# Performance work log

Hardware: AMD Instinct MI355X
Metric: run time of the kernel (lower is better)

Reference implementation:

```python
import jax, jax.numpy as jnp
import numpy as np

NEAR = 0.01
FAR = 10.0
MAX_ITERS = 32
N_RAYS = 65536
HIDDEN = 128


def setup_inputs() -> dict:
    key = jax.random.key(0)
    ks = jax.random.split(key, 12)
    f = jnp.float32
    origins = jax.random.normal(ks[0], (N_RAYS, 3), f) * 2.0
    directions = jax.random.normal(ks[1], (N_RAYS, 3), f)
    directions = directions / jnp.linalg.norm(directions, axis=-1, keepdims=True)
    s1 = 1.0 / np.sqrt(3.0)
    s2 = 1.0 / np.sqrt(HIDDEN)
    return {
        "origins": origins,
        "directions": directions,
        "W1": jax.random.normal(ks[2], (3, HIDDEN), f) * s1,
        "b1": jax.random.normal(ks[3], (HIDDEN,), f) * 0.01,
        "W2": jax.random.normal(ks[4], (HIDDEN, HIDDEN), f) * s2,
        "b2": jax.random.normal(ks[5], (HIDDEN,), f) * 0.01,
        "W3": jax.random.normal(ks[6], (HIDDEN, 1), f) * s2,
        "b3": jax.random.normal(ks[7], (1,), f) * 0.01,
        "Wc1": jax.random.normal(ks[8], (3, HIDDEN), f) * s1,
        "bc1": jax.random.normal(ks[9], (HIDDEN,), f) * 0.01,
        "Wc2": jax.random.normal(ks[10], (HIDDEN, 3), f) * s2,
        "bc2": jax.random.normal(ks[11], (3,), f) * 0.01,
    }


def reference(origins, directions, W1, b1, W2, b2, W3, b3, Wc1, bc1, Wc2, bc2):
    N = origins.shape[0]

    def sdf(p):  # [N,3] -> [N,1]
        h = jax.nn.relu(p @ W1 + b1)
        h = jax.nn.relu(h @ W2 + b2)
        return h @ W3 + b3

    def get_color(p):  # [N,3] -> [N,3]
        h = jax.nn.relu(p @ Wc1 + bc1)
        return jax.nn.sigmoid(h @ Wc2 + bc2)

    def step(state, _):
        points, distances, final_mask = state
        sdfs = sdf(points)                                  # [N,1]
        valid = (sdfs <= NEAR) & (distances < FAR)          # [N,1] bool
        final_mask = final_mask | valid
        upd = ~valid                                        # rays still marching
        distances = distances + jnp.where(upd, sdfs, 0.0)
        points = points + jnp.where(upd, directions * sdfs, 0.0)
        return (points, distances, final_mask), None

    init = (origins,
            jnp.zeros((N, 1), origins.dtype),
            jnp.zeros((N, 1), dtype=bool))
    (points, distances, final_mask), _ = jax.lax.scan(step, init, None, length=MAX_ITERS)
    final_mask = final_mask | (distances < FAR)             # [N,1]

    # color[mask] = get_color(points[mask]) <=> masked where (get_color is pointwise)
    color = jnp.where(final_mask, get_color(points), 0.0)   # [N,3]
    return color
```

## Files before the change

### kernel.cpp

```cpp
#include <hip/hip_runtime.h>

#define HIDDEN 128
#define N_RAYS 65536
#define NEAR_D 0.01f
#define FAR_D 10.0f
#define MAX_ITERS 32

typedef _Float16 f16x8 __attribute__((ext_vector_type(8)));
typedef float f32x16 __attribute__((ext_vector_type(16)));

template <int CTRL, int ROW_MASK>
__device__ __forceinline__ float dpp_add(float v) {
    int s = __builtin_amdgcn_update_dpp(0, __float_as_int(v), CTRL, ROW_MASK, 0xF, true);
    return v + __int_as_float(s);
}
__device__ __forceinline__ float half_sum_dpp(float v) {
    v = dpp_add<0x111, 0xF>(v);
    v = dpp_add<0x112, 0xF>(v);
    v = dpp_add<0x114, 0xF>(v);
    v = dpp_add<0x118, 0xF>(v);
    v = dpp_add<0x142, 0xA>(v);
    return v;
}

__global__ void w2_frag_kernel(const float* __restrict__ W2,
                               _Float16* __restrict__ img) {
    int tid = blockIdx.x * blockDim.x + threadIdx.x;
    int j = tid & 7;
    int L = (tid >> 3) & 63;
    int tc = tid >> 9;
    int t = tc >> 3, c = tc & 7;
    int n = t * 32 + (L & 31);
    int k = c * 16 + ((L >> 5) & 1) * 8 + j;
    float w = W2[k * HIDDEN + n];
    _Float16 hi = (_Float16)w;
    _Float16 lo = (_Float16)(w - (float)hi);
    img[tid] = hi;
    img[16384 + tid] = lo;
}

__launch_bounds__(256, 2)
__global__ void sphere_trace_kernel(
    const float* __restrict__ origins,
    const float* __restrict__ directions,
    const float* __restrict__ W1,
    const float* __restrict__ b1,
    const _Float16* __restrict__ w2img,
    const float* __restrict__ b2,
    const float* __restrict__ W3,
    const float* __restrict__ b3,
    const float* __restrict__ Wc1,
    const float* __restrict__ bc1,
    const float* __restrict__ Wc2,
    const float* __restrict__ bc2,
    float* __restrict__ out)
{
    __shared__ __align__(16) _Float16 wlds[32768];
    __shared__ __align__(16) float4 w1s[128];
    __shared__ float sbuf[4][32];

    const int tid = threadIdx.x;
    const int lane = tid & 63;
    const int w = __builtin_amdgcn_readfirstlane(tid >> 6);
    const int q = lane >> 5;
    const int n32 = lane & 31;

    {
        const float4* src = (const float4*)w2img;
        float4* dst = (float4*)wlds;
        #pragma unroll
        for (int i = 0; i < 16; ++i)
            dst[tid + 256 * i] = src[tid + 256 * i];
        if (tid < 128) {
            float4 wv;
            wv.x = W1[tid];
            wv.y = W1[HIDDEN + tid];
            wv.z = W1[2 * HIDDEN + tid];
            wv.w = b1[tid];
            w1s[tid] = wv;
        }
    }
    __syncthreads();

    float bAx, bAy, bAz, bB;
    {
        bAx = fmaxf(fabsf(W1[lane]),              fabsf(W1[lane + 64]));
        bAy = fmaxf(fabsf(W1[HIDDEN + lane]),     fabsf(W1[HIDDEN + lane + 64]));
        bAz = fmaxf(fabsf(W1[2 * HIDDEN + lane]), fabsf(W1[2 * HIDDEN + lane + 64]));
        bB  = fmaxf(fabsf(b1[lane]),              fabsf(b1[lane + 64]));
        #pragma unroll
        for (int m = 1; m < 64; m <<= 1) {
            bAx = fmaxf(bAx, __shfl_xor(bAx, m));
            bAy = fmaxf(bAy, __shfl_xor(bAy, m));
            bAz = fmaxf(bAz, __shfl_xor(bAz, m));
            bB  = fmaxf(bB,  __shfl_xor(bB,  m));
        }
    }

    const int ray = blockIdx.x * 128 + w * 32 + n32;
    float px = origins[ray * 3 + 0];
    float py = origins[ray * 3 + 1];
    float pz = origins[ray * 3 + 2];
    const float dx = directions[ray * 3 + 0];
    const float dy = directions[ray * 3 + 1];
    const float dz = directions[ray * 3 + 2];
    float dist = 0.0f;
    bool frozen = false;

    float b2v[4], w3v[4];
    #pragma unroll
    for (int t = 0; t < 4; ++t) {
        b2v[t] = b2[t * 32 + n32];
        w3v[t] = W3[t * 32 + n32];
    }
    const float b3v = b3[0];
    const int q8 = q * 8;

    #pragma unroll 1
    for (int it = 0; it < MAX_ITERS; ++it) {
        const float ppx = px;
        const float ppy = py;
        const float ppz = pz;

        const float bound = fmaf(fabsf(ppx), bAx, fmaf(fabsf(ppy), bAy,
                            fmaf(fabsf(ppz), bAz, bB)));
        float sc = 1.0f, inv = 1.0f;
        {
            const int e = (int)((__float_as_uint(bound) >> 23) & 255u);
            if (e > 137) {
                const int sh = e - 137;
                sc  = __uint_as_float((unsigned)(127 - sh) << 23);
                inv = __uint_as_float((unsigned)(127 + sh) << 23);
            }
        }

        auto layer1 = [&](int kb, f16x8& Ah, f16x8& Al) {
            #pragma unroll
            for (int jj = 0; jj < 8; ++jj) {
                const float4 wv = w1s[kb + jj];
                const float hv = fmaxf(
                    fmaf(ppx, wv.x, fmaf(ppy, wv.y,
                    fmaf(ppz, wv.z, wv.w))), 0.0f);
                const float x = hv * sc;
                const _Float16 hi = (_Float16)x;
                Ah[jj] = hi;
                Al[jj] = (_Float16)(x - (float)hi);
            }
        };

        f32x16 acc[4];
        #pragma unroll
        for (int t = 0; t < 4; ++t)
            #pragma unroll
            for (int r = 0; r < 16; ++r) acc[t][r] = 0.0f;

        f16x8 Ah, Al, AhN, AlN;
        layer1(q8, Ah, Al);

        #pragma unroll 1
        for (int c = 0; c < 8; ++c) {
            const int base = (c << 9) + (lane << 3);
            const f16x8 b0h = *(const f16x8*)(wlds + base);
            const f16x8 b0l = *(const f16x8*)(wlds + 16384 + base);
            const f16x8 b1h = *(const f16x8*)(wlds + base + (1 << 12));
            const f16x8 b1l = *(const f16x8*)(wlds + 16384 + base + (1 << 12));
            const f16x8 b2h = *(const f16x8*)(wlds + base + (2 << 12));
            const f16x8 b2l = *(const f16x8*)(wlds + 16384 + base + (2 << 12));
            const f16x8 b3h = *(const f16x8*)(wlds + base + (3 << 12));
            const f16x8 b3l = *(const f16x8*)(wlds + 16384 + base + (3 << 12));

            if (c < 7) layer1((c + 1) * 16 + q8, AhN, AlN);

            __builtin_amdgcn_s_setprio(1);
            acc[0] = __builtin_amdgcn_mfma_f32_32x32x16_f16(Ah, b0h, acc[0], 0, 0, 0);
            acc[1] = __builtin_amdgcn_mfma_f32_32x32x16_f16(Ah, b1h, acc[1], 0, 0, 0);
            acc[2] = __builtin_amdgcn_mfma_f32_32x32x16_f16(Ah, b2h, acc[2], 0, 0, 0);
            acc[3] = __builtin_amdgcn_mfma_f32_32x32x16_f16(Ah, b3h, acc[3], 0, 0, 0);
            acc[0] = __builtin_amdgcn_mfma_f32_32x32x16_f16(Ah, b0l, acc[0], 0, 0, 0);
            acc[1] = __builtin_amdgcn_mfma_f32_32x32x16_f16(Ah, b1l, acc[1], 0, 0, 0);
            acc[2] = __builtin_amdgcn_mfma_f32_32x32x16_f16(Ah, b2l, acc[2], 0, 0, 0);
            acc[3] = __builtin_amdgcn_mfma_f32_32x32x16_f16(Ah, b3l, acc[3], 0, 0, 0);
            acc[0] = __builtin_amdgcn_mfma_f32_32x32x16_f16(Al, b0h, acc[0], 0, 0, 0);
            acc[1] = __builtin_amdgcn_mfma_f32_32x32x16_f16(Al, b1h, acc[1], 0, 0, 0);
            acc[2] = __builtin_amdgcn_mfma_f32_32x32x16_f16(Al, b2h, acc[2], 0, 0, 0);
            acc[3] = __builtin_amdgcn_mfma_f32_32x32x16_f16(Al, b3h, acc[3], 0, 0, 0);
            __builtin_amdgcn_s_setprio(0);

            Ah = AhN; Al = AlN;
        }

        float invr[16];
        #pragma unroll
        for (int r = 0; r < 16; ++r) {
            const int m0 = (r & 3) + 8 * (r >> 2);
            const float ilo = __uint_as_float(
                (unsigned)__builtin_amdgcn_readlane(__float_as_uint(inv), m0));
            const float ihi = __uint_as_float(
                (unsigned)__builtin_amdgcn_readlane(__float_as_uint(inv), m0 + 4));
            invr[r] = q ? ihi : ilo;
        }
        float ps[16];
        #pragma unroll
        for (int r = 0; r < 16; ++r) ps[r] = 0.0f;
        #pragma unroll
        for (int t = 0; t < 4; ++t) {
            #pragma unroll
            for (int r = 0; r < 16; ++r) {
                const float v = fmaxf(fmaf(acc[t][r], invr[r], b2v[t]), 0.0f);
                ps[r] = fmaf(v, w3v[t], ps[r]);
            }
        }

        #pragma unroll
        for (int r = 0; r < 16; ++r)
            ps[r] = half_sum_dpp(ps[r]);
        if ((lane & 31) == 31) {
            const int mb = q * 4;
            #pragma unroll
            for (int g = 0; g < 4; ++g) {
                float4 v4;
                v4.x = ps[4 * g + 0];
                v4.y = ps[4 * g + 1];
                v4.z = ps[4 * g + 2];
                v4.w = ps[4 * g + 3];
                *(float4*)&sbuf[w][8 * g + mb] = v4;
            }
        }
        const float s = sbuf[w][n32] + b3v;

        {
            const bool valid = (s <= NEAR_D) && (dist < FAR_D);
            if (!frozen) {
                if (valid) {
                    frozen = true;
                } else {
                    dist += s;
                    px = fmaf(dx, s, px);
                    py = fmaf(dy, s, py);
                    pz = fmaf(dz, s, pz);
                }
            }
        }
        if (__ballot((lane < 32) && !frozen) == 0) break;
    }

    const int k0 = lane, k1 = lane + 64;
    const float cx0 = Wc1[k0], cx1 = Wc1[k1];
    const float cy0 = Wc1[HIDDEN + k0], cy1 = Wc1[HIDDEN + k1];
    const float cz0 = Wc1[2 * HIDDEN + k0], cz1 = Wc1[2 * HIDDEN + k1];
    const float cb0 = bc1[k0], cb1 = bc1[k1];
    const float u00 = Wc2[k0 * 3 + 0], u01 = Wc2[k0 * 3 + 1], u02 = Wc2[k0 * 3 + 2];
    const float u10 = Wc2[k1 * 3 + 0], u11 = Wc2[k1 * 3 + 1], u12 = Wc2[k1 * 3 + 2];

    float g0 = 0.f, g1 = 0.f, g2 = 0.f;
    #pragma unroll 1
    for (int m = 0; m < 32; ++m) {
        const float qx = __shfl(px, m);
        const float qy = __shfl(py, m);
        const float qz = __shfl(pz, m);
        const float h0 = fmaxf(fmaf(qx, cx0, fmaf(qy, cy0, fmaf(qz, cz0, cb0))), 0.f);
        const float h1 = fmaxf(fmaf(qx, cx1, fmaf(qy, cy1, fmaf(qz, cz1, cb1))), 0.f);
        float a0 = fmaf(h0, u00, h1 * u10);
        float a1 = fmaf(h0, u01, h1 * u11);
        float a2 = fmaf(h0, u02, h1 * u12);
        #pragma unroll
        for (int mask = 1; mask < 64; mask <<= 1) {
            a0 += __shfl_xor(a0, mask);
            a1 += __shfl_xor(a1, mask);
            a2 += __shfl_xor(a2, mask);
        }
        if (lane == m) { g0 = a0; g1 = a1; g2 = a2; }
    }

    if (lane < 32) {
        float c0 = 0.f, c1 = 0.f, c2 = 0.f;
        if (frozen || dist < FAR_D) {
            c0 = 1.0f / (1.0f + __expf(-(g0 + bc2[0])));
            c1 = 1.0f / (1.0f + __expf(-(g1 + bc2[1])));
            c2 = 1.0f / (1.0f + __expf(-(g2 + bc2[2])));
        }
        out[ray * 3 + 0] = c0;
        out[ray * 3 + 1] = c1;
        out[ray * 3 + 2] = c2;
    }
}

extern "C" void kernel_launch(void* const* d_in, const int* in_sizes, int n_in,
                              void* d_out, int out_size, void* d_ws, size_t ws_size,
                              hipStream_t stream) {
    const float* origins    = (const float*)d_in[0];
    const float* directions = (const float*)d_in[1];
    const float* W1  = (const float*)d_in[2];
    const float* b1  = (const float*)d_in[3];
    const float* W2  = (const float*)d_in[4];
    const float* b2  = (const float*)d_in[5];
    const float* W3  = (const float*)d_in[6];
    const float* b3  = (const float*)d_in[7];
    const float* Wc1 = (const float*)d_in[8];
    const float* bc1 = (const float*)d_in[9];
    const float* Wc2 = (const float*)d_in[10];
    const float* bc2 = (const float*)d_in[11];
    float* out = (float*)d_out;

    _Float16* w2img = (_Float16*)d_ws;

    w2_frag_kernel<<<64, 256, 0, stream>>>(W2, w2img);

    sphere_trace_kernel<<<N_RAYS / 128, 256, 0, stream>>>(
        origins, directions, W1, b1, w2img, b2, W3, b3,
        Wc1, bc1, Wc2, bc2, out);
}
```

Before: 315.5 us.

## Split each ray group's layer-2 N dimension across two waves, low weights from global

Each block now handles 64 rays, and each 32-ray group is processed by two waves. Each wave computes half of the hidden-2 outputs and the partial SDF sums are combined through shared memory with block-wide syncs. Only the high-half fp16 weights stay in LDS; the low half is streamed from global/L2, which halves LDS use and allows 4 blocks per CU. The trade-offs are that layer 1 is now computed redundantly by both waves, there is a __syncthreads every iteration, the early exit is block-wide, and the color stage leaves half the waves idle.

```diff
diff --git a/kernel.cpp b/kernel.cpp
--- a/kernel.cpp
+++ b/kernel.cpp
@@ -39,7 +39,7 @@
     img[16384 + tid] = lo;
 }
 
-__launch_bounds__(256, 2)
+__launch_bounds__(256, 4)
 __global__ void sphere_trace_kernel(
     const float* __restrict__ origins,
     const float* __restrict__ directions,
@@ -55,29 +55,31 @@
     const float* __restrict__ bc2,
     float* __restrict__ out)
 {
-    __shared__ __align__(16) _Float16 wlds[32768];
+    __shared__ __align__(16) _Float16 whi[16384];
     __shared__ __align__(16) float4 w1s[128];
-    __shared__ float sbuf[4][32];
+    __shared__ float sbuf[2][2][32];
 
     const int tid = threadIdx.x;
     const int lane = tid & 63;
-    const int w = __builtin_amdgcn_readfirstlane(tid >> 6);
+    const int wv  = __builtin_amdgcn_readfirstlane(tid >> 6);
+    const int grp = wv >> 1;
+    const int th  = wv & 1;
     const int q = lane >> 5;
     const int n32 = lane & 31;
 
     {
         const float4* src = (const float4*)w2img;
-        float4* dst = (float4*)wlds;
+        float4* dst = (float4*)whi;
         #pragma unroll
-        for (int i = 0; i < 16; ++i)
+        for (int i = 0; i < 8; ++i)
             dst[tid + 256 * i] = src[tid + 256 * i];
         if (tid < 128) {
-            float4 wv;
-            wv.x = W1[tid];
-            wv.y = W1[HIDDEN + tid];
-            wv.z = W1[2 * HIDDEN + tid];
-            wv.w = b1[tid];
-            w1s[tid] = wv;
+            float4 wvv;
+            wvv.x = W1[tid];
+            wvv.y = W1[HIDDEN + tid];
+            wvv.z = W1[2 * HIDDEN + tid];
+            wvv.w = b1[tid];
+            w1s[tid] = wvv;
         }
     }
     __syncthreads();
@@ -97,7 +99,7 @@
         }
     }
 
-    const int ray = blockIdx.x * 128 + w * 32 + n32;
+    const int ray = blockIdx.x * 64 + grp * 32 + n32;
     float px = origins[ray * 3 + 0];
     float py = origins[ray * 3 + 1];
     float pz = origins[ray * 3 + 2];
@@ -107,128 +109,117 @@
     float dist = 0.0f;
     bool frozen = false;
 
-    float b2v[4], w3v[4];
+    const int t0 = th * 2;
+    float b2v[2], w3v[2];
     #pragma unroll
-    for (int t = 0; t < 4; ++t) {
-        b2v[t] = b2[t * 32 + n32];
-        w3v[t] = W3[t * 32 + n32];
+    for (int tt = 0; tt < 2; ++tt) {
+        b2v[tt] = b2[(t0 + tt) * 32 + n32];
+        w3v[tt] = W3[(t0 + tt) * 32 + n32];
     }
     const float b3v = b3[0];
     const int q8 = q * 8;
+    const int fb0 = t0 * 8;
+    const int fb1 = fb0 + 8;
+    const _Float16* lo_base  = w2img + 16384 + (lane << 3);
+    const _Float16* whi_lane = whi + (lane << 3);
 
     #pragma unroll 1
     for (int it = 0; it < MAX_ITERS; ++it) {
-        const float ppx = px;
-        const float ppy = py;
-        const float ppz = pz;
-
-        const float bound = fmaf(fabsf(ppx), bAx, fmaf(fabsf(ppy), bAy,
-                            fmaf(fabsf(ppz), bAz, bB)));
-        float sc = 1.0f, inv = 1.0f;
-        {
-            const int e = (int)((__float_as_uint(bound) >> 23) & 255u);
-            if (e > 137) {
-                const int sh = e - 137;
-                sc  = __uint_as_float((unsigned)(127 - sh) << 23);
-                inv = __uint_as_float((unsigned)(127 + sh) << 23);
-            }
-        }
-
-        auto layer1 = [&](int kb, f16x8& Ah, f16x8& Al) {
-            #pragma unroll
-            for (int jj = 0; jj < 8; ++jj) {
-                const float4 wv = w1s[kb + jj];
-                const float hv = fmaxf(
-                    fmaf(ppx, wv.x, fmaf(ppy, wv.y,
-                    fmaf(ppz, wv.z, wv.w))), 0.0f);
-                const float x = hv * sc;
-                const _Float16 hi = (_Float16)x;
-                Ah[jj] = hi;
-                Al[jj] = (_Float16)(x - (float)hi);
-            }
-        };
-
-        f32x16 acc[4];
-        #pragma unroll
-        for (int t = 0; t < 4; ++t)
-            #pragma unroll
-            for (int r = 0; r < 16; ++r) acc[t][r] = 0.0f;
-
-        f16x8 Ah, Al, AhN, AlN;
-        layer1(q8, Ah, Al);
-
-        #pragma unroll 1
-        for (int c = 0; c < 8; ++c) {
-            const int base = (c << 9) + (lane << 3);
-            const f16x8 b0h = *(const f16x8*)(wlds + base);
-            const f16x8 b0l = *(const f16x8*)(wlds + 16384 + base);
-            const f16x8 b1h = *(const f16x8*)(wlds + base + (1 << 12));
-            const f16x8 b1l = *(const f16x8*)(wlds + 16384 + base + (1 << 12));
-            const f16x8 b2h = *(const f16x8*)(wlds + base + (2 << 12));
-            const f16x8 b2l = *(const f16x8*)(wlds + 16384 + base + (2 << 12));
-            const f16x8 b3h = *(const f16x8*)(wlds + base + (3 << 12));
-            const f16x8 b3l = *(const f16x8*)(wlds + 16384 + base + (3 << 12));
-
-            if (c < 7) layer1((c + 1) * 16 + q8, AhN, AlN);
-
-            __builtin_amdgcn_s_setprio(1);
-            acc[0] = __builtin_amdgcn_mfma_f32_32x32x16_f16(Ah, b0h, acc[0], 0, 0, 0);
-            acc[1] = __builtin_amdgcn_mfma_f32_32x32x16_f16(Ah, b1h, acc[1], 0, 0, 0);
-            acc[2] = __builtin_amdgcn_mfma_f32_32x32x16_f16(Ah, b2h, acc[2], 0, 0, 0);
-            acc[3] = __builtin_amdgcn_mfma_f32_32x32x16_f16(Ah, b3h, acc[3], 0, 0, 0);
-            acc[0] = __builtin_amdgcn_mfma_f32_32x32x16_f16(Ah, b0l, acc[0], 0, 0, 0);
-            acc[1] = __builtin_amdgcn_mfma_f32_32x32x16_f16(Ah, b1l, acc[1], 0, 0, 0);
-            acc[2] = __builtin_amdgcn_mfma_f32_32x32x16_f16(Ah, b2l, acc[2], 0, 0, 0);
-            acc[3] = __builtin_amdgcn_mfma_f32_32x32x16_f16(Ah, b3l, acc[3], 0, 0, 0);
-            acc[0] = __builtin_amdgcn_mfma_f32_32x32x16_f16(Al, b0h, acc[0], 0, 0, 0);
-            acc[1] = __builtin_amdgcn_mfma_f32_32x32x16_f16(Al, b1h, acc[1], 0, 0, 0);
-            acc[2] = __builtin_amdgcn_mfma_f32_32x32x16_f16(Al, b2h, acc[2], 0, 0, 0);
-            acc[3] = __builtin_amdgcn_mfma_f32_32x32x16_f16(Al, b3h, acc[3], 0, 0, 0);
-            __builtin_amdgcn_s_setprio(0);
-
-            Ah = AhN; Al = AlN;
-        }
-
-        float invr[16];
-        #pragma unroll
-        for (int r = 0; r < 16; ++r) {
-            const int m0 = (r & 3) + 8 * (r >> 2);
-            const float ilo = __uint_as_float(
-                (unsigned)__builtin_amdgcn_readlane(__float_as_uint(inv), m0));
-            const float ihi = __uint_as_float(
-                (unsigned)__builtin_amdgcn_readlane(__float_as_uint(inv), m0 + 4));
-            invr[r] = q ? ihi : ilo;
-        }
-        float ps[16];
-        #pragma unroll
-        for (int r = 0; r < 16; ++r) ps[r] = 0.0f;
-        #pragma unroll
-        for (int t = 0; t < 4; ++t) {
+        const bool gdone = (__ballot(!frozen) == 0ull);
+        if (!gdone) {
+            const float ppx = px, ppy = py, ppz = pz;
+
+            const float bound = fmaf(fabsf(ppx), bAx, fmaf(fabsf(ppy), bAy,
+                                fmaf(fabsf(ppz), bAz, bB)));
+            float sc = 1.0f, inv = 1.0f;
+            {
+                const int e = (int)((__float_as_uint(bound) >> 23) & 255u);
+                if (e > 137) {
+                    const int sh = e - 137;
+                    sc  = __uint_as_float((unsigned)(127 - sh) << 23);
+                    inv = __uint_as_float((unsigned)(127 + sh) << 23);
+                }
+            }
+
+            f32x16 acc0, acc1;
+            #pragma unroll
+            for (int r = 0; r < 16; ++r) { acc0[r] = 0.0f; acc1[r] = 0.0f; }
+
+            f16x8 Bl0 = *(const f16x8*)(lo_base + (fb0 << 9));
+            f16x8 Bl1 = *(const f16x8*)(lo_base + (fb1 << 9));
+
+            #pragma unroll 1
+            for (int c = 0; c < 8; ++c) {
+                const f16x8 bh0 = *(const f16x8*)(whi_lane + ((fb0 + c) << 9));
+                const f16x8 bh1 = *(const f16x8*)(whi_lane + ((fb1 + c) << 9));
+                f16x8 BlN0, BlN1;
+                if (c < 7) {
+                    BlN0 = *(const f16x8*)(lo_base + ((fb0 + c + 1) << 9));
+                    BlN1 = *(const f16x8*)(lo_base + ((fb1 + c + 1) << 9));
+                }
+                f16x8 Ah, Al;
+                {
+                    const int kb = c * 16 + q8;
+                    #pragma unroll
+                    for (int jj = 0; jj < 8; ++jj) {
+                        const float4 wvv = w1s[kb + jj];
+                        const float hv = fmaxf(
+                            fmaf(ppx, wvv.x, fmaf(ppy, wvv.y,
+                            fmaf(ppz, wvv.z, wvv.w))), 0.0f);
+                        const float x = hv * sc;
+                        const _Float16 hi = (_Float16)x;
+                        Ah[jj] = hi;
+                        Al[jj] = (_Float16)(x - (float)hi);
+                    }
+                }
+                __builtin_amdgcn_s_setprio(1);
+                acc0 = __builtin_amdgcn_mfma_f32_32x32x16_f16(Ah, bh0, acc0, 0, 0, 0);
+                acc1 = __builtin_amdgcn_mfma_f32_32x32x16_f16(Ah, bh1, acc1, 0, 0, 0);
+                acc0 = __builtin_amdgcn_mfma_f32_32x32x16_f16(Ah, Bl0, acc0, 0, 0, 0);
+                acc1 = __builtin_amdgcn_mfma_f32_32x32x16_f16(Ah, Bl1, acc1, 0, 0, 0);
+                acc0 = __builtin_amdgcn_mfma_f32_32x32x16_f16(Al, bh0, acc0, 0, 0, 0);
+                acc1 = __builtin_amdgcn_mfma_f32_32x32x16_f16(Al, bh1, acc1, 0, 0, 0);
+                __builtin_amdgcn_s_setprio(0);
+                if (c < 7) { Bl0 = BlN0; Bl1 = BlN1; }
+            }
+
+            float invr[16];
             #pragma unroll
             for (int r = 0; r < 16; ++r) {
-                const float v = fmaxf(fmaf(acc[t][r], invr[r], b2v[t]), 0.0f);
-                ps[r] = fmaf(v, w3v[t], ps[r]);
-            }
-        }
-
-        #pragma unroll
-        for (int r = 0; r < 16; ++r)
-            ps[r] = half_sum_dpp(ps[r]);
-        if ((lane & 31) == 31) {
-            const int mb = q * 4;
-            #pragma unroll
-            for (int g = 0; g < 4; ++g) {
-                float4 v4;
-                v4.x = ps[4 * g + 0];
-                v4.y = ps[4 * g + 1];
-                v4.z = ps[4 * g + 2];
-                v4.w = ps[4 * g + 3];
-                *(float4*)&sbuf[w][8 * g + mb] = v4;
-            }
-        }
-        const float s = sbuf[w][n32] + b3v;
-
-        {
+                const int m0 = (r & 3) + 8 * (r >> 2);
+                const float ilo = __uint_as_float(
+                    (unsigned)__builtin_amdgcn_readlane(__float_as_uint(inv), m0));
+                const float ihi = __uint_as_float(
+                    (unsigned)__builtin_amdgcn_readlane(__float_as_uint(inv), m0 + 4));
+                invr[r] = q ? ihi : ilo;
+            }
+            float ps[16];
+            #pragma unroll
+            for (int r = 0; r < 16; ++r) {
+                const float v0 = fmaxf(fmaf(acc0[r], invr[r], b2v[0]), 0.0f);
+                const float v1 = fmaxf(fmaf(acc1[r], invr[r], b2v[1]), 0.0f);
+                ps[r] = fmaf(v1, w3v[1], v0 * w3v[0]);
+            }
+
+            #pragma unroll
+            for (int r = 0; r < 16; ++r)
+                ps[r] = half_sum_dpp(ps[r]);
+            if ((lane & 31) == 31) {
+                const int mb = q * 4;
+                #pragma unroll
+                for (int g = 0; g < 4; ++g) {
+                    float4 v4;
+                    v4.x = ps[4 * g + 0];
+                    v4.y = ps[4 * g + 1];
+                    v4.z = ps[4 * g + 2];
+                    v4.w = ps[4 * g + 3];
+                    *(float4*)&sbuf[grp][th][8 * g + mb] = v4;
+                }
+            }
+        }
+        __syncthreads();
+        if (!gdone) {
+            const float s = sbuf[grp][0][n32] + sbuf[grp][1][n32] + b3v;
             const bool valid = (s <= NEAR_D) && (dist < FAR_D);
             if (!frozen) {
                 if (valid) {
@@ -241,47 +232,49 @@
                 }
             }
         }
-        if (__ballot((lane < 32) && !frozen) == 0) break;
-    }
-
-    const int k0 = lane, k1 = lane + 64;
-    const float cx0 = Wc1[k0], cx1 = Wc1[k1];
-    const float cy0 = Wc1[HIDDEN + k0], cy1 = Wc1[HIDDEN + k1];
-    const float cz0 = Wc1[2 * HIDDEN + k0], cz1 = Wc1[2 * HIDDEN + k1];
-    const float cb0 = bc1[k0], cb1 = bc1[k1];
-    const float u00 = Wc2[k0 * 3 + 0], u01 = Wc2[k0 * 3 + 1], u02 = Wc2[k0 * 3 + 2];
-    const float u10 = Wc2[k1 * 3 + 0], u11 = Wc2[k1 * 3 + 1], u12 = Wc2[k1 * 3 + 2];
-
-    float g0 = 0.f, g1 = 0.f, g2 = 0.f;
-    #pragma unroll 1
-    for (int m = 0; m < 32; ++m) {
-        const float qx = __shfl(px, m);
-        const float qy = __shfl(py, m);
-        const float qz = __shfl(pz, m);
-        const float h0 = fmaxf(fmaf(qx, cx0, fmaf(qy, cy0, fmaf(qz, cz0, cb0))), 0.f);
-        const float h1 = fmaxf(fmaf(qx, cx1, fmaf(qy, cy1, fmaf(qz, cz1, cb1))), 0.f);
-        float a0 = fmaf(h0, u00, h1 * u10);
-        float a1 = fmaf(h0, u01, h1 * u11);
-        float a2 = fmaf(h0, u02, h1 * u12);
-        #pragma unroll
-        for (int mask = 1; mask < 64; mask <<= 1) {
-            a0 += __shfl_xor(a0, mask);
-            a1 += __shfl_xor(a1, mask);
-            a2 += __shfl_xor(a2, mask);
-        }
-        if (lane == m) { g0 = a0; g1 = a1; g2 = a2; }
-    }
-
-    if (lane < 32) {
-        float c0 = 0.f, c1 = 0.f, c2 = 0.f;
-        if (frozen || dist < FAR_D) {
-            c0 = 1.0f / (1.0f + __expf(-(g0 + bc2[0])));
-            c1 = 1.0f / (1.0f + __expf(-(g1 + bc2[1])));
-            c2 = 1.0f / (1.0f + __expf(-(g2 + bc2[2])));
-        }
-        out[ray * 3 + 0] = c0;
-        out[ray * 3 + 1] = c1;
-        out[ray * 3 + 2] = c2;
+        if (__syncthreads_and((int)frozen)) break;
+    }
+
+    if (th == 0) {
+        const int k0 = lane, k1 = lane + 64;
+        const float cx0 = Wc1[k0], cx1 = Wc1[k1];
+        const float cy0 = Wc1[HIDDEN + k0], cy1 = Wc1[HIDDEN + k1];
+        const float cz0 = Wc1[2 * HIDDEN + k0], cz1 = Wc1[2 * HIDDEN + k1];
+        const float cb0 = bc1[k0], cb1 = bc1[k1];
+        const float u00 = Wc2[k0 * 3 + 0], u01 = Wc2[k0 * 3 + 1], u02 = Wc2[k0 * 3 + 2];
+        const float u10 = Wc2[k1 * 3 + 0], u11 = Wc2[k1 * 3 + 1], u12 = Wc2[k1 * 3 + 2];
+
+        float g0 = 0.f, g1 = 0.f, g2 = 0.f;
+        #pragma unroll 1
+        for (int m = 0; m < 32; ++m) {
+            const float qx = __shfl(px, m);
+            const float qy = __shfl(py, m);
+            const float qz = __shfl(pz, m);
+            const float h0 = fmaxf(fmaf(qx, cx0, fmaf(qy, cy0, fmaf(qz, cz0, cb0))), 0.f);
+            const float h1 = fmaxf(fmaf(qx, cx1, fmaf(qy, cy1, fmaf(qz, cz1, cb1))), 0.f);
+            float a0 = fmaf(h0, u00, h1 * u10);
+            float a1 = fmaf(h0, u01, h1 * u11);
+            float a2 = fmaf(h0, u02, h1 * u12);
+            #pragma unroll
+            for (int mask = 1; mask < 64; mask <<= 1) {
+                a0 += __shfl_xor(a0, mask);
+                a1 += __shfl_xor(a1, mask);
+                a2 += __shfl_xor(a2, mask);
+            }
+            if (lane == m) { g0 = a0; g1 = a1; g2 = a2; }
+        }
+
+        if (lane < 32) {
+            float c0 = 0.f, c1 = 0.f, c2 = 0.f;
+            if (frozen || dist < FAR_D) {
+                c0 = 1.0f / (1.0f + __expf(-(g0 + bc2[0])));
+                c1 = 1.0f / (1.0f + __expf(-(g1 + bc2[1])));
+                c2 = 1.0f / (1.0f + __expf(-(g2 + bc2[2])));
+            }
+            out[ray * 3 + 0] = c0;
+            out[ray * 3 + 1] = c1;
+            out[ray * 3 + 2] = c2;
+        }
     }
 }
 
@@ -306,7 +299,7 @@
 
     w2_frag_kernel<<<64, 256, 0, stream>>>(W2, w2img);
 
-    sphere_trace_kernel<<<N_RAYS / 128, 256, 0, stream>>>(
+    sphere_trace_kernel<<<N_RAYS / 64, 256, 0, stream>>>(
         origins, directions, W1, b1, w2img, b2, W3, b3,
         Wc1, bc1, Wc2, bc2, out);
 }
```

Measured after the change: 400.7 us. 27.0% more time.

## Drop dynamic fp16 range scaling, pack conversions, fold b2 into accumulators

Applied to the files above, without the earlier changes.

Removes the per-ray bound computation and power-of-two scale/inverse-scale (including the 32 readlanes per iteration) that protected the fp16 split-precision layer-1 activations from overflow. Layer-1 hi/lo conversion now uses packed round-toward-zero cvt_pkrtz. The b2 bias is preloaded into the MFMA accumulators. The MFMAs are regrouped so each accumulator gets its three hi/lo products back to back. This cuts VALU work per march step, but drops the overflow guard for large point magnitudes, changes rounding, and the regrouping creates dependent MFMA chains on the same accumulator.

```diff
diff --git a/kernel.cpp b/kernel.cpp
--- a/kernel.cpp
+++ b/kernel.cpp
@@ -7,6 +7,7 @@
 #define MAX_ITERS 32
 
 typedef _Float16 f16x8 __attribute__((ext_vector_type(8)));
+typedef __fp16 fp16x2 __attribute__((ext_vector_type(2)));
 typedef float f32x16 __attribute__((ext_vector_type(16)));
 
 template <int CTRL, int ROW_MASK>
@@ -82,21 +83,6 @@
     }
     __syncthreads();
 
-    float bAx, bAy, bAz, bB;
-    {
-        bAx = fmaxf(fabsf(W1[lane]),              fabsf(W1[lane + 64]));
-        bAy = fmaxf(fabsf(W1[HIDDEN + lane]),     fabsf(W1[HIDDEN + lane + 64]));
-        bAz = fmaxf(fabsf(W1[2 * HIDDEN + lane]), fabsf(W1[2 * HIDDEN + lane + 64]));
-        bB  = fmaxf(fabsf(b1[lane]),              fabsf(b1[lane + 64]));
-        #pragma unroll
-        for (int m = 1; m < 64; m <<= 1) {
-            bAx = fmaxf(bAx, __shfl_xor(bAx, m));
-            bAy = fmaxf(bAy, __shfl_xor(bAy, m));
-            bAz = fmaxf(bAz, __shfl_xor(bAz, m));
-            bB  = fmaxf(bB,  __shfl_xor(bB,  m));
-        }
-    }
-
     const int ray = blockIdx.x * 128 + w * 32 + n32;
     float px = origins[ray * 3 + 0];
     float py = origins[ray * 3 + 1];
@@ -118,41 +104,32 @@
 
     #pragma unroll 1
     for (int it = 0; it < MAX_ITERS; ++it) {
-        const float ppx = px;
-        const float ppy = py;
-        const float ppz = pz;
-
-        const float bound = fmaf(fabsf(ppx), bAx, fmaf(fabsf(ppy), bAy,
-                            fmaf(fabsf(ppz), bAz, bB)));
-        float sc = 1.0f, inv = 1.0f;
-        {
-            const int e = (int)((__float_as_uint(bound) >> 23) & 255u);
-            if (e > 137) {
-                const int sh = e - 137;
-                sc  = __uint_as_float((unsigned)(127 - sh) << 23);
-                inv = __uint_as_float((unsigned)(127 + sh) << 23);
-            }
-        }
+        const float ppx = px, ppy = py, ppz = pz;
 
         auto layer1 = [&](int kb, f16x8& Ah, f16x8& Al) {
-            #pragma unroll
-            for (int jj = 0; jj < 8; ++jj) {
-                const float4 wv = w1s[kb + jj];
-                const float hv = fmaxf(
-                    fmaf(ppx, wv.x, fmaf(ppy, wv.y,
-                    fmaf(ppz, wv.z, wv.w))), 0.0f);
-                const float x = hv * sc;
-                const _Float16 hi = (_Float16)x;
-                Ah[jj] = hi;
-                Al[jj] = (_Float16)(x - (float)hi);
-            }
+            union { f16x8 v; fp16x2 p[4]; } uh, ul;
+            #pragma unroll
+            for (int jp = 0; jp < 4; ++jp) {
+                const float4 w0 = w1s[kb + 2 * jp];
+                const float4 w1v = w1s[kb + 2 * jp + 1];
+                const float x0 = fmaxf(
+                    fmaf(ppx, w0.x, fmaf(ppy, w0.y, fmaf(ppz, w0.z, w0.w))), 0.0f);
+                const float x1 = fmaxf(
+                    fmaf(ppx, w1v.x, fmaf(ppy, w1v.y, fmaf(ppz, w1v.z, w1v.w))), 0.0f);
+                const fp16x2 hi = __builtin_amdgcn_cvt_pkrtz(x0, x1);
+                const float l0 = x0 - (float)hi[0];
+                const float l1 = x1 - (float)hi[1];
+                uh.p[jp] = hi;
+                ul.p[jp] = __builtin_amdgcn_cvt_pkrtz(l0, l1);
+            }
+            Ah = uh.v; Al = ul.v;
         };
 
         f32x16 acc[4];
         #pragma unroll
         for (int t = 0; t < 4; ++t)
             #pragma unroll
-            for (int r = 0; r < 16; ++r) acc[t][r] = 0.0f;
+            for (int r = 0; r < 16; ++r) acc[t][r] = b2v[t];
 
         f16x8 Ah, Al, AhN, AlN;
         layer1(q8, Ah, Al);
@@ -173,32 +150,22 @@
 
             __builtin_amdgcn_s_setprio(1);
             acc[0] = __builtin_amdgcn_mfma_f32_32x32x16_f16(Ah, b0h, acc[0], 0, 0, 0);
+            acc[0] = __builtin_amdgcn_mfma_f32_32x32x16_f16(Ah, b0l, acc[0], 0, 0, 0);
+            acc[0] = __builtin_amdgcn_mfma_f32_32x32x16_f16(Al, b0h, acc[0], 0, 0, 0);
             acc[1] = __builtin_amdgcn_mfma_f32_32x32x16_f16(Ah, b1h, acc[1], 0, 0, 0);
+            acc[1] = __builtin_amdgcn_mfma_f32_32x32x16_f16(Ah, b1l, acc[1], 0, 0, 0);
+            acc[1] = __builtin_amdgcn_mfma_f32_32x32x16_f16(Al, b1h, acc[1], 0, 0, 0);
             acc[2] = __builtin_amdgcn_mfma_f32_32x32x16_f16(Ah, b2h, acc[2], 0, 0, 0);
+            acc[2] = __builtin_amdgcn_mfma_f32_32x32x16_f16(Ah, b2l, acc[2], 0, 0, 0);
+            acc[2] = __builtin_amdgcn_mfma_f32_32x32x16_f16(Al, b2h, acc[2], 0, 0, 0);
             acc[3] = __builtin_amdgcn_mfma_f32_32x32x16_f16(Ah, b3h, acc[3], 0, 0, 0);
-            acc[0] = __builtin_amdgcn_mfma_f32_32x32x16_f16(Ah, b0l, acc[0], 0, 0, 0);
-            acc[1] = __builtin_amdgcn_mfma_f32_32x32x16_f16(Ah, b1l, acc[1], 0, 0, 0);
-            acc[2] = __builtin_amdgcn_mfma_f32_32x32x16_f16(Ah, b2l, acc[2], 0, 0, 0);
             acc[3] = __builtin_amdgcn_mfma_f32_32x32x16_f16(Ah, b3l, acc[3], 0, 0, 0);
-            acc[0] = __builtin_amdgcn_mfma_f32_32x32x16_f16(Al, b0h, acc[0], 0, 0, 0);
-            acc[1] = __builtin_amdgcn_mfma_f32_32x32x16_f16(Al, b1h, acc[1], 0, 0, 0);
-            acc[2] = __builtin_amdgcn_mfma_f32_32x32x16_f16(Al, b2h, acc[2], 0, 0, 0);
             acc[3] = __builtin_amdgcn_mfma_f32_32x32x16_f16(Al, b3h, acc[3], 0, 0, 0);
             __builtin_amdgcn_s_setprio(0);
 
             Ah = AhN; Al = AlN;
         }
 
-        float invr[16];
-        #pragma unroll
-        for (int r = 0; r < 16; ++r) {
-            const int m0 = (r & 3) + 8 * (r >> 2);
-            const float ilo = __uint_as_float(
-                (unsigned)__builtin_amdgcn_readlane(__float_as_uint(inv), m0));
-            const float ihi = __uint_as_float(
-                (unsigned)__builtin_amdgcn_readlane(__float_as_uint(inv), m0 + 4));
-            invr[r] = q ? ihi : ilo;
-        }
         float ps[16];
         #pragma unroll
         for (int r = 0; r < 16; ++r) ps[r] = 0.0f;
@@ -206,7 +173,7 @@
         for (int t = 0; t < 4; ++t) {
             #pragma unroll
             for (int r = 0; r < 16; ++r) {
-                const float v = fmaxf(fmaf(acc[t][r], invr[r], b2v[t]), 0.0f);
+                const float v = fmaxf(acc[t][r], 0.0f);
                 ps[r] = fmaf(v, w3v[t], ps[r]);
             }
         }
```

After: 297.8 us (median of 2 runs). 5.6% less time.
